# Kernel optimization log

Measured on AMD Instinct MI355X. Metric: run time of the kernel, lower is better.

Reference implementation:

```python
import jax, jax.numpy as jnp
import numpy as np

NEG_INF = -1e30

def setup_inputs() -> dict:
    key = jax.random.key(0)
    k1, k2, k3, k4, k5 = jax.random.split(key, 5)
    B, N, Fin, Fout, H = 8, 1024, 128, 64, 4
    h = jax.random.normal(k1, (B, N, Fin), dtype=jnp.float32)
    adj = jax.random.randint(k2, (N, N), 0, 2, dtype=jnp.int32)
    bias_matrix = jax.random.normal(k3, (1, 1, N, N), dtype=jnp.float32)
    # xavier-ish scaled params
    W = jax.random.normal(k4, (H, Fin, Fout), dtype=jnp.float32) * (1.0 / np.sqrt(Fin))
    a = jax.random.normal(k5, (H, 2 * Fout, 1), dtype=jnp.float32) * (1.0 / np.sqrt(2 * Fout))
    return {"h": h, "adj": adj, "bias_matrix": bias_matrix, "W": W, "a": a}


def reference(h, adj, bias_matrix, W, a):
    B, N, _ = h.shape
    H, _, Fout = W.shape
    # h_prime: [B, N, H, Fout]
    h_prime = jnp.einsum('bni,hio->bnho', h, W)
    # split attention vector: a_input @ a == h_i @ a1 + h_j @ a2 (same math, no O(N^2*F) tensor)
    a1 = a[:, :Fout, 0]   # [H, Fout]
    a2 = a[:, Fout:, 0]   # [H, Fout]
    ei = jnp.einsum('bnhf,hf->bnh', h_prime, a1)  # [B, N, H]
    ej = jnp.einsum('bnhf,hf->bnh', h_prime, a2)  # [B, N, H]
    e = jax.nn.leaky_relu(ei[:, :, None, :] + ej[:, None, :, :], negative_slope=0.2)  # [B,N,N,H]
    # bias_matrix [1,1,N,N] -> expand to [B,1,N,N] -> permute(0,2,3,1) -> [B,N,N,1]
    bias = jnp.transpose(bias_matrix, (0, 2, 3, 1))  # [1, N, N, 1], broadcasts to [B,N,N,H]
    e = e + bias
    mask = (adj != 0)[None, :, :, None]  # [1, N, N, 1]
    e_masked = jnp.where(mask, e, NEG_INF)
    attention = jax.nn.softmax(e_masked, axis=2)  # softmax over j
    h_out = jnp.einsum('bijh,bjhf->bihf', attention, h_prime)  # [B, N, H, Fout]
    return h_out.reshape(B, N, H * Fout)
```

## Files before the change

kernel.cpp:

```cpp
#include <hip/hip_runtime.h>

constexpr int B = 8, N = 1024, FIN = 128, FOUT = 64, H = 4;
constexpr float LOG2E = 1.44269504f;

typedef __attribute__((ext_vector_type(8))) short short8;
typedef __attribute__((ext_vector_type(4))) short short4v;
typedef __attribute__((ext_vector_type(4))) float f32x4;

static __device__ inline unsigned short f2bf(float x) {
    union { float f; unsigned u; } v; v.f = x;
    unsigned r = v.u + 0x7fff + ((v.u >> 16) & 1);
    return (unsigned short)(r >> 16);
}

__global__ __launch_bounds__(256) void gat_prep(
    const float* __restrict__ h,
    const float* __restrict__ W,
    const float* __restrict__ a,
    const int*   __restrict__ adj,
    const float* __restrict__ bias,
    unsigned short* __restrict__ hpF,
    unsigned short* __restrict__ mbB,
    float* __restrict__ ei_t,
    float* __restrict__ ej_t)
{
    __shared__ float h_lds[16][132];
    const int t = threadIdx.x;

    if (blockIdx.x < 512) {
        const int bx   = blockIdx.x;
        const int ti   = bx >> 3;
        const int jc   = (bx & 7) * 4 + (t >> 6);
        const int lane = t & 63;
        const int i    = ti * 16 + (lane & 15);
        const int j0   = jc * 32 + 8 * (lane >> 4);

        const int4*   ap = reinterpret_cast<const int4*>(adj + (size_t)i * N + j0);
        const float4* bp = reinterpret_cast<const float4*>(bias + (size_t)i * N + j0);
        int4   a0 = ap[0], a1 = ap[1];
        float4 b0 = bp[0], b1 = bp[1];
        unsigned short q0 = f2bf(a0.x ? LOG2E * b0.x : -1e35f);
        unsigned short q1 = f2bf(a0.y ? LOG2E * b0.y : -1e35f);
        unsigned short q2 = f2bf(a0.z ? LOG2E * b0.z : -1e35f);
        unsigned short q3 = f2bf(a0.w ? LOG2E * b0.w : -1e35f);
        unsigned short q4 = f2bf(a1.x ? LOG2E * b1.x : -1e35f);
        unsigned short q5 = f2bf(a1.y ? LOG2E * b1.y : -1e35f);
        unsigned short q6 = f2bf(a1.z ? LOG2E * b1.z : -1e35f);
        unsigned short q7 = f2bf(a1.w ? LOG2E * b1.w : -1e35f);
        int4 ov;
        ov.x = (int)((unsigned)q0 | ((unsigned)q1 << 16));
        ov.y = (int)((unsigned)q2 | ((unsigned)q3 << 16));
        ov.z = (int)((unsigned)q4 | ((unsigned)q5 << 16));
        ov.w = (int)((unsigned)q6 | ((unsigned)q7 << 16));
        *reinterpret_cast<int4*>(mbB + (((size_t)ti * 32 + jc) * 64 + lane) * 8) = ov;
        return;
    }

    const int blk = blockIdx.x - 512;
    const int b   = blk >> 6;
    const int n0  = (blk & 63) * 16;

    {
        const float* src = h + ((size_t)b * N + n0) * FIN;
        for (int v = t; v < 512; v += 256) {
            float4 x = reinterpret_cast<const float4*>(src)[v];
            int fl = v * 4;
            *reinterpret_cast<float4*>(&h_lds[fl >> 7][fl & 127]) = x;
        }
    }
    __syncthreads();

    const int hd   = t >> 6;
    const int lane = t & 63;
    const int li   = lane & 15;
    const int f0   = li * 4;
    const int rg   = lane >> 4;

    float acc[4][4];
    #pragma unroll
    for (int k = 0; k < 4; ++k)
        #pragma unroll
        for (int j = 0; j < 4; ++j) acc[k][j] = 0.f;

    const float* Wp = W + (size_t)hd * FIN * FOUT + f0;
    #pragma unroll 8
    for (int i = 0; i < FIN; ++i) {
        float4 w4 = *reinterpret_cast<const float4*>(Wp + (size_t)i * FOUT);
        #pragma unroll
        for (int k = 0; k < 4; ++k) {
            float hv = h_lds[4 * rg + k][i];
            acc[k][0] = fmaf(hv, w4.x, acc[k][0]);
            acc[k][1] = fmaf(hv, w4.y, acc[k][1]);
            acc[k][2] = fmaf(hv, w4.z, acc[k][2]);
            acc[k][3] = fmaf(hv, w4.w, acc[k][3]);
        }
    }

    const int bh = b * H + hd;
    {
        const int na  = n0 + 4 * rg;
        const int jc  = na >> 5;
        const int kgn = (na >> 3) & 3;
        const int ft  = li >> 2;
        const int e0  = na & 4;
        #pragma unroll
        for (int jj = 0; jj < 4; ++jj) {
            short4v v4;
            v4[0] = (short)f2bf(acc[0][jj]);
            v4[1] = (short)f2bf(acc[1][jj]);
            v4[2] = (short)f2bf(acc[2][jj]);
            v4[3] = (short)f2bf(acc[3][jj]);
            const int lanep = (4 * (li & 3) + jj) + 16 * kgn;
            *reinterpret_cast<short4v*>(
                hpF + ((((size_t)bh * 32 + jc) * 4 + ft) * 64 + lanep) * 8 + e0) = v4;
        }
    }

    float4 a1 = *reinterpret_cast<const float4*>(a + (size_t)hd * 2 * FOUT + f0);
    float4 a2 = *reinterpret_cast<const float4*>(a + (size_t)hd * 2 * FOUT + FOUT + f0);
    #pragma unroll
    for (int k = 0; k < 4; ++k) {
        float e1 = acc[k][0] * a1.x + acc[k][1] * a1.y + acc[k][2] * a1.z + acc[k][3] * a1.w;
        float e2 = acc[k][0] * a2.x + acc[k][1] * a2.y + acc[k][2] * a2.z + acc[k][3] * a2.w;
        #pragma unroll
        for (int m = 1; m < 16; m <<= 1) {
            e1 += __shfl_xor(e1, m, 64);
            e2 += __shfl_xor(e2, m, 64);
        }
        if (li == 0) {
            int r = n0 + 4 * rg + k;
            ei_t[(size_t)bh * N + r] = LOG2E * e1;
            ej_t[(size_t)bh * N + r] = LOG2E * e2;
        }
    }
}

__global__ __launch_bounds__(512) void gat_attn(
    const unsigned short* __restrict__ hpF,
    const float* __restrict__ ei_t,
    const float* __restrict__ ej_t,
    const unsigned short* __restrict__ mbB,
    float* __restrict__ out)
{
    __shared__ __align__(16) char smem[32768];
    typedef unsigned short hstage_t[2][4][512];
    hstage_t* hstage = reinterpret_cast<hstage_t*>(smem);

    const int raw  = blockIdx.x;
    const int xcd  = raw & 7;
    const int k_   = raw >> 3;
    const int bh   = ((xcd >> 1) << 3) | (k_ >> 3);
    const int it0  = (((xcd & 1) << 3) | (k_ & 7)) * 4;
    const int t    = threadIdx.x;
    const int w8   = t >> 6;
    const int w    = w8 & 3;
    const int jh   = w8 >> 2;
    const int lane = t & 63;
    const int li   = lane & 15;
    const int kg   = lane >> 4;
    const int ti   = it0 + w;
    const int irow = ti * 16 + li;
    const int jcb  = jh * 16;

    const float  ei0   = ei_t[(size_t)bh * N + irow];
    const float* ejrow = ej_t + (size_t)bh * N;
    const unsigned short* mrow = mbB + ((size_t)ti * 32 * 64 + lane) * 8;
    const size_t hbase = (size_t)bh * 65536;

    f32x4 c0 = {0.f,0.f,0.f,0.f}, c1 = {0.f,0.f,0.f,0.f};
    f32x4 c2 = {0.f,0.f,0.f,0.f}, c3 = {0.f,0.f,0.f,0.f};
    f32x4 c4 = {0.f,0.f,0.f,0.f};
    const short obf = (short)0x3F80;
    const short8 ones = {obf,obf,obf,obf,obf,obf,obf,obf};

    #define VMCNT6() asm volatile("s_waitcnt vmcnt(6)" ::: "memory")
    #define BARRIER() { __builtin_amdgcn_s_barrier(); asm volatile("" ::: "memory"); }

    #define STAGE(BUF, JCG) {                                                 \
        const unsigned short* gs_ = hpF + hbase + (size_t)(JCG) * 2048        \
                                        + (size_t)w * 512 + (size_t)lane * 8; \
        __builtin_amdgcn_global_load_lds(                                     \
            (const __attribute__((address_space(1))) void*)gs_,               \
            (__attribute__((address_space(3))) void*)&hstage[BUF][jh][w][0],  \
            16, 0, 0); }

    #define REGS(S, JCG) {                                                    \
        mq##S  = *reinterpret_cast<const int4*>(mrow + (size_t)(JCG) * 512);  \
        ejA##S = *reinterpret_cast<const float4*>(ejrow + (JCG) * 32 + 8 * kg);\
        ejB##S = *reinterpret_cast<const float4*>(ejrow + (JCG) * 32 + 8 * kg + 4); }

    #define DSREAD(BUF, BA, BB, BC, BD) {                                     \
        BA = *reinterpret_cast<const short8*>(&hstage[BUF][jh][0][lane * 8]); \
        BB = *reinterpret_cast<const short8*>(&hstage[BUF][jh][1][lane * 8]); \
        BC = *reinterpret_cast<const short8*>(&hstage[BUF][jh][2][lane * 8]); \
        BD = *reinterpret_cast<const short8*>(&hstage[BUF][jh][3][lane * 8]); }

    #define SCORE2(PL, PH, EJL, EJH, QW) {                                    \
        float bl_ = __uint_as_float(((unsigned)(QW)) << 16);                  \
        float bh_ = __uint_as_float(((unsigned)(QW)) & 0xffff0000u);          \
        float el_ = ei0 + (EJL); el_ = fmaxf(el_, 0.2f * el_) + bl_;          \
        float eh_ = ei0 + (EJH); eh_ = fmaxf(eh_, 0.2f * eh_) + bh_;          \
        asm("v_exp_f32 %0, %1" : "=v"(PL) : "v"(el_));                        \
        asm("v_exp_f32 %0, %1" : "=v"(PH) : "v"(eh_)); }

    #define COMPS(S, BA, BB, BC, BD) {                                        \
        float p0,p1,p2,p3,p4,p5,p6,p7;                                        \
        SCORE2(p0, p1, ejA##S.x, ejA##S.y, mq##S.x)                           \
        SCORE2(p2, p3, ejA##S.z, ejA##S.w, mq##S.y)                           \
        SCORE2(p4, p5, ejB##S.x, ejB##S.y, mq##S.z)                           \
        SCORE2(p6, p7, ejB##S.z, ejB##S.w, mq##S.w)                           \
        int4 pk_;                                                             \
        asm("v_cvt_pk_bf16_f32 %0, %1, %2" : "=v"(pk_.x) : "v"(p0), "v"(p1)); \
        asm("v_cvt_pk_bf16_f32 %0, %1, %2" : "=v"(pk_.y) : "v"(p2), "v"(p3)); \
        asm("v_cvt_pk_bf16_f32 %0, %1, %2" : "=v"(pk_.z) : "v"(p4), "v"(p5)); \
        asm("v_cvt_pk_bf16_f32 %0, %1, %2" : "=v"(pk_.w) : "v"(p6), "v"(p7)); \
        short8 a0_ = *reinterpret_cast<short8*>(&pk_);                        \
        c0 = __builtin_amdgcn_mfma_f32_16x16x32_bf16(a0_, BA, c0, 0, 0, 0);   \
        c1 = __builtin_amdgcn_mfma_f32_16x16x32_bf16(a0_, BB, c1, 0, 0, 0);   \
        c2 = __builtin_amdgcn_mfma_f32_16x16x32_bf16(a0_, BC, c2, 0, 0, 0);   \
        c3 = __builtin_amdgcn_mfma_f32_16x16x32_bf16(a0_, BD, c3, 0, 0, 0);   \
        c4 = __builtin_amdgcn_mfma_f32_16x16x32_bf16(a0_, ones, c4, 0, 0, 0); }

    short8 A0, B0, C0, D0, A1, B1, C1, D1;
    int4 mq0, mq1;
    float4 ejA0, ejB0, ejA1, ejB1;

    STAGE(0, jcb + 0)
    STAGE(1, jcb + 1)
    REGS(0, jcb + 0)
    REGS(1, jcb + 1)
    VMCNT6();
    BARRIER();

    #pragma unroll 1
    for (int k = 0; k < 16; k += 2) {
        const int pa = (k + 2 < 16) ? jcb + k + 2 : jcb + 15;
        const int pb = (k + 3 < 16) ? jcb + k + 3 : jcb + 15;
        const int ba = k & 2 ? 2 : 0;
        const int bb = ba + 1;
        const int bn0 = ba ^ 2;
        const int bn1 = bb ^ 2;
        STAGE(bn0, pa)
        STAGE(bn1, pb)
        DSREAD(ba, A0, B0, C0, D0)
        COMPS(0, A0, B0, C0, D0)
        REGS(0, pa)
        DSREAD(bb, A1, B1, C1, D1)
        COMPS(1, A1, B1, C1, D1)
        REGS(1, pb)
        VMCNT6();
        BARRIER();
    }
    #undef VMCNT6
    #undef BARRIER
    #undef STAGE
    #undef REGS
    #undef DSREAD
    #undef SCORE2
    #undef COMPS

    f32x4 (*red)[4][64] = reinterpret_cast<f32x4 (*)[4][64]>(smem);

    __syncthreads();
    if (jh == 1) {
        red[0][w][lane] = c0;
        red[1][w][lane] = c1;
        red[2][w][lane] = c2;
        red[3][w][lane] = c3;
        red[4][w][lane] = c4;
    }
    __syncthreads();
    if (jh == 1) return;

    c0 += red[0][w][lane];
    c1 += red[1][w][lane];
    c2 += red[2][w][lane];
    c3 += red[3][w][lane];
    c4 += red[4][w][lane];

    const int b  = bh >> 2;
    const int hd = bh & 3;
    #pragma unroll
    for (int r = 0; r < 4; ++r) {
        int orow = ti * 16 + 4 * kg + r;
        float inv = 1.0f / c4[r];
        float* ob = out + (((size_t)b * N + orow) * H + hd) * 64 + li;
        ob[0]  = c0[r] * inv;
        ob[16] = c1[r] * inv;
        ob[32] = c2[r] * inv;
        ob[48] = c3[r] * inv;
    }
}

extern "C" void kernel_launch(void* const* d_in, const int* in_sizes, int n_in,
                              void* d_out, int out_size, void* d_ws, size_t ws_size,
                              hipStream_t stream) {
    const float* h    = (const float*)d_in[0];
    const int*   adj  = (const int*)  d_in[1];
    const float* bias = (const float*)d_in[2];
    const float* W    = (const float*)d_in[3];
    const float* a    = (const float*)d_in[4];
    float* out = (float*)d_out;

    char* ws = (char*)d_ws;
    unsigned short* hpF = (unsigned short*)ws;
    unsigned short* mbB = (unsigned short*)(ws + ((size_t)4 << 20));
    float* ei_t = (float*)(ws + ((size_t)6 << 20));
    float* ej_t = ei_t + (size_t)B * H * N;

    gat_prep<<<512 + B * N / 16, 256, 0, stream>>>(h, W, a, adj, bias,
                                                   hpF, mbB, ei_t, ej_t);
    gat_attn<<<B * H * (N / 64), 512, 0, stream>>>(hpF, ei_t, ej_t, mbB, out);
}
```

Baseline: 35.24 us.

## Compute h·W projection in prep kernel with bf16 MFMA instead of scalar FMA

Replaces the scalar FP32 FMA loop for the h·W projection with bf16 16x16x32 MFMA instructions. W fragments are loaded and converted into registers while the h tile is staged in LDS. Each block now covers 32 rows instead of 16, which halves the number of projection blocks. The result layout and the ei/ej reductions are rewritten to match the MFMA output mapping. The attention logits ei/ej were previously computed from fp32 projections and are now computed from bf16-rounded inputs, which adds some precision loss.

```diff
diff --git a/kernel.cpp b/kernel.cpp
--- a/kernel.cpp
+++ b/kernel.cpp
@@ -24,7 +24,7 @@
     float* __restrict__ ei_t,
     float* __restrict__ ej_t)
 {
-    __shared__ float h_lds[16][132];
+    __shared__ float h_lds[32][132];
     const int t = threadIdx.x;
 
     if (blockIdx.x < 512) {
@@ -57,82 +57,110 @@
     }
 
     const int blk = blockIdx.x - 512;
-    const int b   = blk >> 6;
-    const int n0  = (blk & 63) * 16;
+    const int b   = blk >> 5;
+    const int n0  = (blk & 31) * 32;
 
     {
         const float* src = h + ((size_t)b * N + n0) * FIN;
-        for (int v = t; v < 512; v += 256) {
+        for (int v = t; v < 1024; v += 256) {
             float4 x = reinterpret_cast<const float4*>(src)[v];
             int fl = v * 4;
             *reinterpret_cast<float4*>(&h_lds[fl >> 7][fl & 127]) = x;
         }
     }
-    __syncthreads();
 
     const int hd   = t >> 6;
     const int lane = t & 63;
     const int li   = lane & 15;
-    const int f0   = li * 4;
-    const int rg   = lane >> 4;
-
-    float acc[4][4];
-    #pragma unroll
-    for (int k = 0; k < 4; ++k)
-        #pragma unroll
-        for (int j = 0; j < 4; ++j) acc[k][j] = 0.f;
-
-    const float* Wp = W + (size_t)hd * FIN * FOUT + f0;
-    #pragma unroll 8
-    for (int i = 0; i < FIN; ++i) {
-        float4 w4 = *reinterpret_cast<const float4*>(Wp + (size_t)i * FOUT);
-        #pragma unroll
-        for (int k = 0; k < 4; ++k) {
-            float hv = h_lds[4 * rg + k][i];
-            acc[k][0] = fmaf(hv, w4.x, acc[k][0]);
-            acc[k][1] = fmaf(hv, w4.y, acc[k][1]);
-            acc[k][2] = fmaf(hv, w4.z, acc[k][2]);
-            acc[k][3] = fmaf(hv, w4.w, acc[k][3]);
+    const int kg   = lane >> 4;
+
+    short8 wf[4][4];
+    {
+        const float* Wp = W + (size_t)hd * FIN * FOUT;
+        #pragma unroll
+        for (int ks = 0; ks < 4; ++ks)
+            #pragma unroll
+            for (int ft = 0; ft < 4; ++ft) {
+                const float* wb = Wp + (size_t)(ks * 32 + 8 * kg) * FOUT + 16 * ft + li;
+                int4 pk_;
+                float u0 = wb[0],       u1 = wb[64],      u2 = wb[128], u3 = wb[192];
+                float u4 = wb[256],     u5 = wb[320],     u6 = wb[384], u7 = wb[448];
+                asm("v_cvt_pk_bf16_f32 %0, %1, %2" : "=v"(pk_.x) : "v"(u0), "v"(u1));
+                asm("v_cvt_pk_bf16_f32 %0, %1, %2" : "=v"(pk_.y) : "v"(u2), "v"(u3));
+                asm("v_cvt_pk_bf16_f32 %0, %1, %2" : "=v"(pk_.z) : "v"(u4), "v"(u5));
+                asm("v_cvt_pk_bf16_f32 %0, %1, %2" : "=v"(pk_.w) : "v"(u6), "v"(u7));
+                wf[ks][ft] = *reinterpret_cast<short8*>(&pk_);
+            }
+    }
+    __syncthreads();
+
+    f32x4 c[4][2];
+    #pragma unroll
+    for (int ft = 0; ft < 4; ++ft)
+        #pragma unroll
+        for (int rt = 0; rt < 2; ++rt) c[ft][rt] = f32x4{0.f, 0.f, 0.f, 0.f};
+
+    #pragma unroll
+    for (int rt = 0; rt < 2; ++rt) {
+        #pragma unroll
+        for (int ks = 0; ks < 4; ++ks) {
+            const float* hp8 = &h_lds[16 * rt + li][ks * 32 + 8 * kg];
+            float4 x0 = *reinterpret_cast<const float4*>(hp8);
+            float4 x1 = *reinterpret_cast<const float4*>(hp8 + 4);
+            int4 pk_;
+            asm("v_cvt_pk_bf16_f32 %0, %1, %2" : "=v"(pk_.x) : "v"(x0.x), "v"(x0.y));
+            asm("v_cvt_pk_bf16_f32 %0, %1, %2" : "=v"(pk_.y) : "v"(x0.z), "v"(x0.w));
+            asm("v_cvt_pk_bf16_f32 %0, %1, %2" : "=v"(pk_.z) : "v"(x1.x), "v"(x1.y));
+            asm("v_cvt_pk_bf16_f32 %0, %1, %2" : "=v"(pk_.w) : "v"(x1.z), "v"(x1.w));
+            short8 af = *reinterpret_cast<short8*>(&pk_);
+            c[0][rt] = __builtin_amdgcn_mfma_f32_16x16x32_bf16(af, wf[ks][0], c[0][rt], 0, 0, 0);
+            c[1][rt] = __builtin_amdgcn_mfma_f32_16x16x32_bf16(af, wf[ks][1], c[1][rt], 0, 0, 0);
+            c[2][rt] = __builtin_amdgcn_mfma_f32_16x16x32_bf16(af, wf[ks][2], c[2][rt], 0, 0, 0);
+            c[3][rt] = __builtin_amdgcn_mfma_f32_16x16x32_bf16(af, wf[ks][3], c[3][rt], 0, 0, 0);
         }
     }
 
     const int bh = b * H + hd;
-    {
-        const int na  = n0 + 4 * rg;
-        const int jc  = na >> 5;
-        const int kgn = (na >> 3) & 3;
-        const int ft  = li >> 2;
-        const int e0  = na & 4;
-        #pragma unroll
-        for (int jj = 0; jj < 4; ++jj) {
+    const int jc = n0 >> 5;
+    #pragma unroll
+    for (int ft = 0; ft < 4; ++ft)
+        #pragma unroll
+        for (int rt = 0; rt < 2; ++rt) {
             short4v v4;
-            v4[0] = (short)f2bf(acc[0][jj]);
-            v4[1] = (short)f2bf(acc[1][jj]);
-            v4[2] = (short)f2bf(acc[2][jj]);
-            v4[3] = (short)f2bf(acc[3][jj]);
-            const int lanep = (4 * (li & 3) + jj) + 16 * kgn;
+            v4[0] = (short)f2bf(c[ft][rt][0]);
+            v4[1] = (short)f2bf(c[ft][rt][1]);
+            v4[2] = (short)f2bf(c[ft][rt][2]);
+            v4[3] = (short)f2bf(c[ft][rt][3]);
+            const int lanep = li + 16 * (2 * rt + (kg >> 1));
             *reinterpret_cast<short4v*>(
-                hpF + ((((size_t)bh * 32 + jc) * 4 + ft) * 64 + lanep) * 8 + e0) = v4;
+                hpF + ((((size_t)bh * 32 + jc) * 4 + ft) * 64 + lanep) * 8 + 4 * (kg & 1)) = v4;
         }
-    }
-
-    float4 a1 = *reinterpret_cast<const float4*>(a + (size_t)hd * 2 * FOUT + f0);
-    float4 a2 = *reinterpret_cast<const float4*>(a + (size_t)hd * 2 * FOUT + FOUT + f0);
-    #pragma unroll
-    for (int k = 0; k < 4; ++k) {
-        float e1 = acc[k][0] * a1.x + acc[k][1] * a1.y + acc[k][2] * a1.z + acc[k][3] * a1.w;
-        float e2 = acc[k][0] * a2.x + acc[k][1] * a2.y + acc[k][2] * a2.z + acc[k][3] * a2.w;
-        #pragma unroll
-        for (int m = 1; m < 16; m <<= 1) {
-            e1 += __shfl_xor(e1, m, 64);
-            e2 += __shfl_xor(e2, m, 64);
+
+    float a1v[4], a2v[4];
+    #pragma unroll
+    for (int ft = 0; ft < 4; ++ft) {
+        a1v[ft] = a[(size_t)hd * 2 * FOUT + 16 * ft + li];
+        a2v[ft] = a[(size_t)hd * 2 * FOUT + FOUT + 16 * ft + li];
+    }
+    #pragma unroll
+    for (int rt = 0; rt < 2; ++rt)
+        #pragma unroll
+        for (int r = 0; r < 4; ++r) {
+            float e1 = c[0][rt][r] * a1v[0] + c[1][rt][r] * a1v[1]
+                     + c[2][rt][r] * a1v[2] + c[3][rt][r] * a1v[3];
+            float e2 = c[0][rt][r] * a2v[0] + c[1][rt][r] * a2v[1]
+                     + c[2][rt][r] * a2v[2] + c[3][rt][r] * a2v[3];
+            #pragma unroll
+            for (int m = 1; m < 16; m <<= 1) {
+                e1 += __shfl_xor(e1, m, 64);
+                e2 += __shfl_xor(e2, m, 64);
+            }
+            if (li == 0) {
+                int rr = n0 + 16 * rt + 4 * kg + r;
+                ei_t[(size_t)bh * N + rr] = LOG2E * e1;
+                ej_t[(size_t)bh * N + rr] = LOG2E * e2;
+            }
         }
-        if (li == 0) {
-            int r = n0 + 4 * rg + k;
-            ei_t[(size_t)bh * N + r] = LOG2E * e1;
-            ej_t[(size_t)bh * N + r] = LOG2E * e2;
-        }
-    }
 }
 
 __global__ __launch_bounds__(512) void gat_attn(
@@ -308,7 +336,7 @@
     float* ei_t = (float*)(ws + ((size_t)6 << 20));
     float* ej_t = ei_t + (size_t)B * H * N;
 
-    gat_prep<<<512 + B * N / 16, 256, 0, stream>>>(h, W, a, adj, bias,
+    gat_prep<<<512 + B * N / 32, 256, 0, stream>>>(h, W, a, adj, bias,
                                                    hpF, mbB, ei_t, ej_t);
     gat_attn<<<B * H * (N / 64), 512, 0, stream>>>(hpF, ei_t, ej_t, mbB, out);
 }
```

Result: no change. 34.71 us (-1.5%).
